# Performance work log

Measured on AMD Instinct MI355X. Metric: run time of the kernel, lower is better.

Reference implementation:

```python
import jax, jax.numpy as jnp
import numpy as np

B, N, D, P = 4, 16384, 128, 100


def setup_inputs() -> dict:
    key = jax.random.key(0)
    k1, k2, k3 = jax.random.split(key, 3)
    x = jax.random.normal(k1, (B, N, D), dtype=jnp.float32)
    y = jax.random.normal(k2, (B, N, D), dtype=jnp.float32)
    thetas = jax.random.normal(k3, (P, D), dtype=jnp.float32)
    return {"x": x, "y": y, "thetas": thetas}


def reference(x, y, thetas):
    # Sliced OT (the branch taken since B*N*N*4 bytes >> memory limit).
    n_proj = thetas.shape[0]
    # F.normalize(theta, dim=0) per projection direction (eps clamp 1e-12)
    norms = jnp.maximum(jnp.linalg.norm(thetas, axis=-1, keepdims=True), 1e-12)
    thetas = thetas / norms  # (P, d)

    # Project all points onto all directions: (P, B, N)
    x_proj = jnp.einsum('bnd,pd->pbn', x, thetas)
    y_proj = jnp.einsum('bnd,pd->pbn', y, thetas)

    # torch: sort y_proj; scatter y_sorted back to original order of x via
    # x_indices = argsort(x_proj). Equivalent: transported_proj[n] =
    # y_sorted[rank_of_x_proj[n]], with rank = argsort(argsort(.)).
    y_sorted = jnp.sort(y_proj, axis=-1)
    ranks = jnp.argsort(jnp.argsort(x_proj, axis=-1), axis=-1)
    transported_proj = jnp.take_along_axis(y_sorted, ranks, axis=-1)  # (P, B, N)

    # Accumulate (transported_proj - x_proj) * theta over projections.
    transported = jnp.einsum('pbn,pd->bnd', transported_proj - x_proj, thetas)
    return x + transported / n_proj
```

## Files before the change

kernel.cpp:

```cpp
#include <hip/hip_runtime.h>
#include <hip/hip_bf16.h>

#define B_    4
#define N_    16384
#define D_    128
#define P_    100
#define BN_   65536
#define PBN_  6553600
#define PPAD  112
#define KPAD  128
#define NBIN  4096

typedef __attribute__((ext_vector_type(8))) short short8;
typedef __attribute__((ext_vector_type(4))) float floatx4;

__device__ __forceinline__ unsigned short f2b(float f) {
    unsigned u = __float_as_uint(f);
    return (unsigned short)((u + 0x7FFFu + ((u >> 16) & 1u)) >> 16);
}
__device__ __forceinline__ float b2f(unsigned short h) {
    return __uint_as_float(((unsigned)h) << 16);
}

__global__ void k_norm(const float* __restrict__ th,
                       unsigned short* __restrict__ thb,
                       unsigned short* __restrict__ thbT) {
    int p = blockIdx.x;
    int d = threadIdx.x;
    float v = 0.f;
    if (p < P_) v = th[p * D_ + d];
    float s = v * v;
    #pragma unroll
    for (int o = 32; o > 0; o >>= 1) s += __shfl_down(s, o, 64);
    __shared__ float red[2];
    if ((d & 63) == 0) red[d >> 6] = s;
    __syncthreads();
    float norm = fmaxf(sqrtf(red[0] + red[1]), 1e-12f);
    unsigned short r = f2b(v / norm);
    if (p < PPAD) thb[p * D_ + d] = r;
    thbT[d * KPAD + p] = r;
}

__global__ __launch_bounds__(256, 4) void k_proj(
    const float* __restrict__ x, const float* __restrict__ y,
    const unsigned short* __restrict__ thb,
    unsigned short* __restrict__ xp, unsigned short* __restrict__ yp) {
    __shared__ unsigned short th_s[15232];
    __shared__ unsigned short buf[4608];
    const int tid  = threadIdx.x;
    const int w    = tid >> 6;
    const int lane = tid & 63;
    const int n    = lane & 15;
    const int quad = lane >> 4;
    const int row0 = blockIdx.x * 64;

    for (int g = tid; g < 1792; g += 256) {
        int r = g >> 4, c = (g & 15) << 3;
        *(uint4*)(th_s + r * 136 + c) = *(const uint4*)(thb + r * D_ + c);
    }

    const float* xr = x + (size_t)(row0 + w * 16 + n) * D_ + quad * 8;
    const float* yr = y + (size_t)(row0 + w * 16 + n) * D_ + quad * 8;
    short8 bx[4], by[4];
    {
        float4 lx[8];
        #pragma unroll
        for (int ks = 0; ks < 4; ++ks) {
            lx[2*ks]   = *(const float4*)(xr + ks * 32);
            lx[2*ks+1] = *(const float4*)(xr + ks * 32 + 4);
        }
        #pragma unroll
        for (int ks = 0; ks < 4; ++ks) {
            short8 t;
            t[0] = (short)f2b(lx[2*ks].x);   t[1] = (short)f2b(lx[2*ks].y);
            t[2] = (short)f2b(lx[2*ks].z);   t[3] = (short)f2b(lx[2*ks].w);
            t[4] = (short)f2b(lx[2*ks+1].x); t[5] = (short)f2b(lx[2*ks+1].y);
            t[6] = (short)f2b(lx[2*ks+1].z); t[7] = (short)f2b(lx[2*ks+1].w);
            bx[ks] = t;
        }
    }
    {
        float4 ly[8];
        #pragma unroll
        for (int ks = 0; ks < 4; ++ks) {
            ly[2*ks]   = *(const float4*)(yr + ks * 32);
            ly[2*ks+1] = *(const float4*)(yr + ks * 32 + 4);
        }
        #pragma unroll
        for (int ks = 0; ks < 4; ++ks) {
            short8 t;
            t[0] = (short)f2b(ly[2*ks].x);   t[1] = (short)f2b(ly[2*ks].y);
            t[2] = (short)f2b(ly[2*ks].z);   t[3] = (short)f2b(ly[2*ks].w);
            t[4] = (short)f2b(ly[2*ks+1].x); t[5] = (short)f2b(ly[2*ks+1].y);
            t[6] = (short)f2b(ly[2*ks+1].z); t[7] = (short)f2b(ly[2*ks+1].w);
            by[ks] = t;
        }
    }
    __syncthreads();

    floatx4 ay[7];

    #pragma unroll
    for (int pt = 0; pt < 4; ++pt) {
        floatx4 accx = {0.f, 0.f, 0.f, 0.f};
        floatx4 accy = {0.f, 0.f, 0.f, 0.f};
        #pragma unroll
        for (int ks = 0; ks < 4; ++ks) {
            short8 a = *(const short8*)(th_s + (pt * 16 + n) * 136 + ks * 32 + quad * 8);
            accx = __builtin_amdgcn_mfma_f32_16x16x32_bf16(a, bx[ks], accx, 0, 0, 0);
            accy = __builtin_amdgcn_mfma_f32_16x16x32_bf16(a, by[ks], accy, 0, 0, 0);
        }
        #pragma unroll
        for (int reg = 0; reg < 4; ++reg)
            buf[(pt * 16 + quad * 4 + reg) * 72 + w * 16 + n] = f2b(accx[reg]);
        ay[pt] = accy;
    }
    __syncthreads();
    for (int g = tid; g < 512; g += 256) {
        int p = g >> 3, c = (g & 7) << 3;
        *(uint4*)(xp + (size_t)p * BN_ + row0 + c) = *(const uint4*)(buf + p * 72 + c);
    }
    __syncthreads();

    #pragma unroll
    for (int pt = 4; pt < 7; ++pt) {
        floatx4 accx = {0.f, 0.f, 0.f, 0.f};
        floatx4 accy = {0.f, 0.f, 0.f, 0.f};
        #pragma unroll
        for (int ks = 0; ks < 4; ++ks) {
            short8 a = *(const short8*)(th_s + (pt * 16 + n) * 136 + ks * 32 + quad * 8);
            accx = __builtin_amdgcn_mfma_f32_16x16x32_bf16(a, bx[ks], accx, 0, 0, 0);
            accy = __builtin_amdgcn_mfma_f32_16x16x32_bf16(a, by[ks], accy, 0, 0, 0);
        }
        #pragma unroll
        for (int reg = 0; reg < 4; ++reg)
            buf[((pt - 4) * 16 + quad * 4 + reg) * 72 + w * 16 + n] = f2b(accx[reg]);
        ay[pt] = accy;
    }
    __syncthreads();
    for (int g = tid; g < 288; g += 256) {
        int p = g >> 3, c = (g & 7) << 3;
        *(uint4*)(xp + (size_t)(64 + p) * BN_ + row0 + c) = *(const uint4*)(buf + p * 72 + c);
    }
    __syncthreads();

    #pragma unroll
    for (int pt = 0; pt < 4; ++pt)
        #pragma unroll
        for (int reg = 0; reg < 4; ++reg)
            buf[(pt * 16 + quad * 4 + reg) * 72 + w * 16 + n] = f2b(ay[pt][reg]);
    __syncthreads();
    for (int g = tid; g < 512; g += 256) {
        int p = g >> 3, c = (g & 7) << 3;
        *(uint4*)(yp + (size_t)p * BN_ + row0 + c) = *(const uint4*)(buf + p * 72 + c);
    }
    __syncthreads();

    #pragma unroll
    for (int pt = 4; pt < 7; ++pt)
        #pragma unroll
        for (int reg = 0; reg < 4; ++reg)
            buf[((pt - 4) * 16 + quad * 4 + reg) * 72 + w * 16 + n] = f2b(ay[pt][reg]);
    __syncthreads();
    for (int g = tid; g < 288; g += 256) {
        int p = g >> 3, c = (g & 7) << 3;
        *(uint4*)(yp + (size_t)(64 + p) * BN_ + row0 + c) = *(const uint4*)(buf + p * 72 + c);
    }
}

__device__ __forceinline__ int binof(float v) {
    int k = (int)((v + 8.0f) * 256.0f);
    return k < 0 ? 0 : (k > NBIN - 1 ? NBIN - 1 : k);
}

__device__ __forceinline__ void scan4(unsigned* hist, volatile unsigned* wsum, int t) {
    unsigned v[4], run = 0;
    #pragma unroll
    for (int i = 0; i < 4; ++i) { unsigned h = hist[t * 4 + i]; v[i] = run; run += h; }
    const int lane = t & 63, w = t >> 6;
    unsigned inc = run;
    #pragma unroll
    for (int off = 1; off < 64; off <<= 1) {
        unsigned nbr = __shfl_up(inc, off, 64);
        if (lane >= off) inc += nbr;
    }
    if (lane == 63) wsum[w] = inc;
    __syncthreads();
    if (t == 0) {
        unsigned r2 = 0;
        #pragma unroll
        for (int i = 0; i < 16; ++i) { unsigned h = wsum[i]; wsum[i] = r2; r2 += h; }
    }
    __syncthreads();
    unsigned base = wsum[w] + (inc - run);
    #pragma unroll
    for (int i = 0; i < 4; ++i) hist[t * 4 + i] = base + v[i];
}

__global__ __launch_bounds__(1024, 8) void k_sortdiff(
    const unsigned short* __restrict__ xp, const unsigned short* __restrict__ yp,
    unsigned short* __restrict__ diff) {
    __shared__ unsigned hist[NBIN];
    __shared__ unsigned short ysort[N_];
    __shared__ unsigned wsum[16];
    const int t = threadIdx.x;
    const unsigned* ypd = (const unsigned*)(yp + (size_t)blockIdx.x * N_);
    const unsigned* xpd = (const unsigned*)(xp + (size_t)blockIdx.x * N_);
    unsigned*       dfd = (unsigned*)(diff + (size_t)blockIdx.x * N_);

    #pragma unroll
    for (int i = 0; i < 4; ++i) hist[t + i * 1024] = 0;
    __syncthreads();

    unsigned jy[8], jx[8];
    #pragma unroll
    for (int i = 0; i < 2; ++i) {
        uint4 a = *(const uint4*)(ypd + i * 4096 + t * 4);
        unsigned aw0 = a.x, aw1 = a.y, aw2 = a.z, aw3 = a.w;
        unsigned aws[4] = {aw0, aw1, aw2, aw3};
        #pragma unroll
        for (int q = 0; q < 4; ++q) {
            unsigned j0 = atomicAdd(&hist[binof(b2f((unsigned short)(aws[q] & 0xffff)))], 1u);
            unsigned j1 = atomicAdd(&hist[binof(b2f((unsigned short)(aws[q] >> 16)))], 1u);
            jy[4*i + q] = (j0 & 0xffffu) | (j1 << 16);
        }
    }
    #pragma unroll
    for (int i = 0; i < 2; ++i) {
        uint4 c = *(const uint4*)(xpd + i * 4096 + t * 4);
        unsigned cw0 = c.x, cw1 = c.y, cw2 = c.z, cw3 = c.w;
        unsigned cws[4] = {cw0, cw1, cw2, cw3};
        #pragma unroll
        for (int q = 0; q < 4; ++q) {
            unsigned i0 = atomicAdd(&hist[binof(b2f((unsigned short)(cws[q] & 0xffff)))], 0x10000u);
            unsigned i1 = atomicAdd(&hist[binof(b2f((unsigned short)(cws[q] >> 16)))], 0x10000u);
            jx[4*i + q] = (i0 >> 16) | (i1 & 0xffff0000u);
        }
    }
    __syncthreads();
    scan4(hist, wsum, t);
    __syncthreads();

    #pragma unroll
    for (int i = 0; i < 2; ++i) {
        uint4 a = *(const uint4*)(ypd + i * 4096 + t * 4);
        unsigned aws[4] = {a.x, a.y, a.z, a.w};
        #pragma unroll
        for (int q = 0; q < 4; ++q) {
            int k = 4*i + q;
            unsigned short e0 = (unsigned short)(aws[q] & 0xffff);
            unsigned short e1 = (unsigned short)(aws[q] >> 16);
            ysort[(hist[binof(b2f(e0))] & 0xffffu) + (jy[k] & 0xffffu)] = e0;
            ysort[(hist[binof(b2f(e1))] & 0xffffu) + (jy[k] >> 16)]     = e1;
        }
    }
    __syncthreads();

    #pragma unroll
    for (int i = 0; i < 2; ++i) {
        uint4 c = *(const uint4*)(xpd + i * 4096 + t * 4);
        unsigned cws[4] = {c.x, c.y, c.z, c.w};
        unsigned o[4];
        #pragma unroll
        for (int q = 0; q < 4; ++q) {
            int k = 4*i + q;
            float x0 = b2f((unsigned short)(cws[q] & 0xffff));
            float x1 = b2f((unsigned short)(cws[q] >> 16));
            unsigned r0 = (hist[binof(x0)] >> 16) + (jx[k] & 0xffffu);
            unsigned r1 = (hist[binof(x1)] >> 16) + (jx[k] >> 16);
            unsigned short d0 = f2b(b2f(ysort[r0]) - x0);
            unsigned short d1 = f2b(b2f(ysort[r1]) - x1);
            o[q] = (unsigned)d0 | ((unsigned)d1 << 16);
        }
        *(uint4*)(dfd + i * 4096 + t * 4) = make_uint4(o[0], o[1], o[2], o[3]);
    }
}

__global__ __launch_bounds__(256, 4) void k_comb(
    const float* __restrict__ x, const unsigned short* __restrict__ diff,
    const unsigned short* __restrict__ thbT, float* __restrict__ out) {
    __shared__ unsigned short ths[64 * 136];
    __shared__ unsigned Lp[64 * 68];
    const int tid  = threadIdx.x;
    const int w    = tid >> 6;
    const int lane = tid & 63;
    const int n16  = lane & 15;
    const int quad = lane >> 4;
    const int row0 = blockIdx.x * 64;

    for (int g = tid; g < 1024; g += 256) {
        int r = g >> 4, c = (g & 15) << 3;
        *(uint4*)(ths + r * 136 + c) = *(const uint4*)(thbT + r * KPAD + c);
    }
    for (int g = tid; g < 952; g += 256) Lp[50 * 68 + g] = 0;
    for (int g = tid; g < 400; g += 256) {
        int p2 = g >> 3, rg = (g & 7) << 3;
        uint4 a = *(const uint4*)(diff + (size_t)(2 * p2) * BN_ + row0 + rg);
        uint4 b = *(const uint4*)(diff + (size_t)(2 * p2 + 1) * BN_ + row0 + rg);
        unsigned* dst = Lp + p2 * 68 + rg;
        dst[0] = (a.x & 0xffffu) | (b.x << 16);
        dst[1] = (a.x >> 16)     | (b.x & 0xffff0000u);
        dst[2] = (a.y & 0xffffu) | (b.y << 16);
        dst[3] = (a.y >> 16)     | (b.y & 0xffff0000u);
        dst[4] = (a.z & 0xffffu) | (b.z << 16);
        dst[5] = (a.z >> 16)     | (b.z & 0xffff0000u);
        dst[6] = (a.w & 0xffffu) | (b.w << 16);
        dst[7] = (a.w >> 16)     | (b.w & 0xffff0000u);
    }
    __syncthreads();

    const int r = w * 16 + n16;
    short8 af[4];
    #pragma unroll
    for (int ks = 0; ks < 4; ++ks) {
        union { unsigned u[4]; short8 v; } tu;
        #pragma unroll
        for (int m = 0; m < 4; ++m)
            tu.u[m] = Lp[(ks * 16 + quad * 4 + m) * 68 + r];
        af[ks] = tu.v;
    }

    const float invP = 1.0f / (float)P_;
    const size_t rbase = (size_t)(row0 + w * 16 + quad * 4) * D_ + n16;

    #pragma unroll
    for (int nt = 0; nt < 4; ++nt) {
        floatx4 acc = {0.f, 0.f, 0.f, 0.f};
        #pragma unroll
        for (int ks = 0; ks < 4; ++ks) {
            short8 b = *(const short8*)(ths + (nt * 16 + n16) * 136 + ks * 32 + quad * 8);
            acc = __builtin_amdgcn_mfma_f32_16x16x32_bf16(af[ks], b, acc, 0, 0, 0);
        }
        #pragma unroll
        for (int reg = 0; reg < 4; ++reg) {
            size_t o = rbase + (size_t)reg * D_ + nt * 16;
            out[o] = fmaf(acc[reg], invP, x[o]);
        }
    }
    __syncthreads();

    for (int g = tid; g < 1024; g += 256) {
        int r2 = g >> 4, c = (g & 15) << 3;
        *(uint4*)(ths + r2 * 136 + c) = *(const uint4*)(thbT + (size_t)(64 + r2) * KPAD + c);
    }
    __syncthreads();

    #pragma unroll
    for (int nt = 0; nt < 4; ++nt) {
        floatx4 acc = {0.f, 0.f, 0.f, 0.f};
        #pragma unroll
        for (int ks = 0; ks < 4; ++ks) {
            short8 b = *(const short8*)(ths + (nt * 16 + n16) * 136 + ks * 32 + quad * 8);
            acc = __builtin_amdgcn_mfma_f32_16x16x32_bf16(af[ks], b, acc, 0, 0, 0);
        }
        #pragma unroll
        for (int reg = 0; reg < 4; ++reg) {
            size_t o = rbase + (size_t)reg * D_ + (64 + nt * 16);
            out[o] = fmaf(acc[reg], invP, x[o]);
        }
    }
}

extern "C" void kernel_launch(void* const* d_in, const int* in_sizes, int n_in,
                              void* d_out, int out_size, void* d_ws, size_t ws_size,
                              hipStream_t stream) {
    const float* x  = (const float*)d_in[0];
    const float* y  = (const float*)d_in[1];
    const float* th = (const float*)d_in[2];
    float* out = (float*)d_out;
    char*  wsb = (char*)d_ws;

    unsigned short* thb  = (unsigned short*)wsb;
    unsigned short* thbT = (unsigned short*)(wsb + 32768);
    unsigned short* xpb  = (unsigned short*)(wsb + 65536);
    unsigned short* ypb  = xpb + PBN_;

    k_norm<<<128, 128, 0, stream>>>(th, thb, thbT);
    k_proj<<<BN_ / 64, 256, 0, stream>>>(x, y, thb, xpb, ypb);
    k_sortdiff<<<P_ * B_, 1024, 0, stream>>>(xpb, ypb, xpb);
    k_comb<<<BN_ / 64, 256, 0, stream>>>(x, xpb, thbT, out);
}
```

Baseline: 138.3 us.

## Fuse theta normalization into projection kernel and drop separate norm launch

New measurement: 143.3 us. 3.6% more time.

```diff
diff --git a/kernel.cpp b/kernel.cpp
--- a/kernel.cpp
+++ b/kernel.cpp
@@ -22,31 +22,13 @@
     return __uint_as_float(((unsigned)h) << 16);
 }
 
-__global__ void k_norm(const float* __restrict__ th,
-                       unsigned short* __restrict__ thb,
-                       unsigned short* __restrict__ thbT) {
-    int p = blockIdx.x;
-    int d = threadIdx.x;
-    float v = 0.f;
-    if (p < P_) v = th[p * D_ + d];
-    float s = v * v;
-    #pragma unroll
-    for (int o = 32; o > 0; o >>= 1) s += __shfl_down(s, o, 64);
-    __shared__ float red[2];
-    if ((d & 63) == 0) red[d >> 6] = s;
-    __syncthreads();
-    float norm = fmaxf(sqrtf(red[0] + red[1]), 1e-12f);
-    unsigned short r = f2b(v / norm);
-    if (p < PPAD) thb[p * D_ + d] = r;
-    thbT[d * KPAD + p] = r;
-}
-
 __global__ __launch_bounds__(256, 4) void k_proj(
     const float* __restrict__ x, const float* __restrict__ y,
-    const unsigned short* __restrict__ thb,
+    const float* __restrict__ th, unsigned short* __restrict__ thbT,
     unsigned short* __restrict__ xp, unsigned short* __restrict__ yp) {
     __shared__ unsigned short th_s[15232];
     __shared__ unsigned short buf[4608];
+    __shared__ float invn[128];
     const int tid  = threadIdx.x;
     const int w    = tid >> 6;
     const int lane = tid & 63;
@@ -54,49 +36,72 @@
     const int quad = lane >> 4;
     const int row0 = blockIdx.x * 64;
 
+    const float* xr = x + (size_t)(row0 + w * 16 + n) * D_ + quad * 8;
+    const float* yr = y + (size_t)(row0 + w * 16 + n) * D_ + quad * 8;
+    float4 lx[8], ly[8];
+    #pragma unroll
+    for (int ks = 0; ks < 4; ++ks) {
+        lx[2*ks]   = *(const float4*)(xr + ks * 32);
+        lx[2*ks+1] = *(const float4*)(xr + ks * 32 + 4);
+        ly[2*ks]   = *(const float4*)(yr + ks * 32);
+        ly[2*ks+1] = *(const float4*)(yr + ks * 32 + 4);
+    }
+
+    {
+        int p = tid >> 1, half = tid & 1;
+        float s = 0.f;
+        if (p < P_) {
+            const float* tr = th + (size_t)p * D_ + half * 64;
+            #pragma unroll
+            for (int i = 0; i < 16; ++i) {
+                float4 v = *(const float4*)(tr + i * 4);
+                s += v.x * v.x + v.y * v.y + v.z * v.z + v.w * v.w;
+            }
+        }
+        s += __shfl_xor(s, 1, 64);
+        if (half == 0 && p < 128)
+            invn[p] = (p < P_) ? 1.f / fmaxf(sqrtf(s), 1e-12f) : 0.f;
+    }
+    __syncthreads();
+
     for (int g = tid; g < 1792; g += 256) {
         int r = g >> 4, c = (g & 15) << 3;
-        *(uint4*)(th_s + r * 136 + c) = *(const uint4*)(thb + r * D_ + c);
-    }
-
-    const float* xr = x + (size_t)(row0 + w * 16 + n) * D_ + quad * 8;
-    const float* yr = y + (size_t)(row0 + w * 16 + n) * D_ + quad * 8;
+        ushort4 lo, hi;
+        if (r < P_) {
+            float sc = invn[r];
+            float4 a = *(const float4*)(th + (size_t)r * D_ + c);
+            float4 b = *(const float4*)(th + (size_t)r * D_ + c + 4);
+            lo = make_ushort4(f2b(a.x * sc), f2b(a.y * sc), f2b(a.z * sc), f2b(a.w * sc));
+            hi = make_ushort4(f2b(b.x * sc), f2b(b.y * sc), f2b(b.z * sc), f2b(b.w * sc));
+        } else {
+            lo = make_ushort4(0, 0, 0, 0);
+            hi = make_ushort4(0, 0, 0, 0);
+        }
+        *(ushort4*)(th_s + r * 136 + c)     = lo;
+        *(ushort4*)(th_s + r * 136 + c + 4) = hi;
+    }
+    __syncthreads();
+
+    if (blockIdx.x < KPAD && tid < KPAD) {
+        int d = blockIdx.x;
+        unsigned short v = (tid < PPAD) ? th_s[tid * 136 + d] : (unsigned short)0;
+        thbT[(size_t)d * KPAD + tid] = v;
+    }
+
     short8 bx[4], by[4];
-    {
-        float4 lx[8];
-        #pragma unroll
-        for (int ks = 0; ks < 4; ++ks) {
-            lx[2*ks]   = *(const float4*)(xr + ks * 32);
-            lx[2*ks+1] = *(const float4*)(xr + ks * 32 + 4);
-        }
-        #pragma unroll
-        for (int ks = 0; ks < 4; ++ks) {
-            short8 t;
-            t[0] = (short)f2b(lx[2*ks].x);   t[1] = (short)f2b(lx[2*ks].y);
-            t[2] = (short)f2b(lx[2*ks].z);   t[3] = (short)f2b(lx[2*ks].w);
-            t[4] = (short)f2b(lx[2*ks+1].x); t[5] = (short)f2b(lx[2*ks+1].y);
-            t[6] = (short)f2b(lx[2*ks+1].z); t[7] = (short)f2b(lx[2*ks+1].w);
-            bx[ks] = t;
-        }
-    }
-    {
-        float4 ly[8];
-        #pragma unroll
-        for (int ks = 0; ks < 4; ++ks) {
-            ly[2*ks]   = *(const float4*)(yr + ks * 32);
-            ly[2*ks+1] = *(const float4*)(yr + ks * 32 + 4);
-        }
-        #pragma unroll
-        for (int ks = 0; ks < 4; ++ks) {
-            short8 t;
-            t[0] = (short)f2b(ly[2*ks].x);   t[1] = (short)f2b(ly[2*ks].y);
-            t[2] = (short)f2b(ly[2*ks].z);   t[3] = (short)f2b(ly[2*ks].w);
-            t[4] = (short)f2b(ly[2*ks+1].x); t[5] = (short)f2b(ly[2*ks+1].y);
-            t[6] = (short)f2b(ly[2*ks+1].z); t[7] = (short)f2b(ly[2*ks+1].w);
-            by[ks] = t;
-        }
-    }
-    __syncthreads();
+    #pragma unroll
+    for (int ks = 0; ks < 4; ++ks) {
+        short8 tx, ty;
+        tx[0] = (short)f2b(lx[2*ks].x);   ty[0] = (short)f2b(ly[2*ks].x);
+        tx[1] = (short)f2b(lx[2*ks].y);   ty[1] = (short)f2b(ly[2*ks].y);
+        tx[2] = (short)f2b(lx[2*ks].z);   ty[2] = (short)f2b(ly[2*ks].z);
+        tx[3] = (short)f2b(lx[2*ks].w);   ty[3] = (short)f2b(ly[2*ks].w);
+        tx[4] = (short)f2b(lx[2*ks+1].x); ty[4] = (short)f2b(ly[2*ks+1].x);
+        tx[5] = (short)f2b(lx[2*ks+1].y); ty[5] = (short)f2b(ly[2*ks+1].y);
+        tx[6] = (short)f2b(lx[2*ks+1].z); ty[6] = (short)f2b(ly[2*ks+1].z);
+        tx[7] = (short)f2b(lx[2*ks+1].w); ty[7] = (short)f2b(ly[2*ks+1].w);
+        bx[ks] = tx; by[ks] = ty;
+    }
 
     floatx4 ay[7];
 
@@ -216,8 +221,7 @@
     #pragma unroll
     for (int i = 0; i < 2; ++i) {
         uint4 a = *(const uint4*)(ypd + i * 4096 + t * 4);
-        unsigned aw0 = a.x, aw1 = a.y, aw2 = a.z, aw3 = a.w;
-        unsigned aws[4] = {aw0, aw1, aw2, aw3};
+        unsigned aws[4] = {a.x, a.y, a.z, a.w};
         #pragma unroll
         for (int q = 0; q < 4; ++q) {
             unsigned j0 = atomicAdd(&hist[binof(b2f((unsigned short)(aws[q] & 0xffff)))], 1u);
@@ -228,8 +232,7 @@
     #pragma unroll
     for (int i = 0; i < 2; ++i) {
         uint4 c = *(const uint4*)(xpd + i * 4096 + t * 4);
-        unsigned cw0 = c.x, cw1 = c.y, cw2 = c.z, cw3 = c.w;
-        unsigned cws[4] = {cw0, cw1, cw2, cw3};
+        unsigned cws[4] = {c.x, c.y, c.z, c.w};
         #pragma unroll
         for (int q = 0; q < 4; ++q) {
             unsigned i0 = atomicAdd(&hist[binof(b2f((unsigned short)(cws[q] & 0xffff)))], 0x10000u);
@@ -370,13 +373,11 @@
     float* out = (float*)d_out;
     char*  wsb = (char*)d_ws;
 
-    unsigned short* thb  = (unsigned short*)wsb;
     unsigned short* thbT = (unsigned short*)(wsb + 32768);
     unsigned short* xpb  = (unsigned short*)(wsb + 65536);
     unsigned short* ypb  = xpb + PBN_;
 
-    k_norm<<<128, 128, 0, stream>>>(th, thb, thbT);
-    k_proj<<<BN_ / 64, 256, 0, stream>>>(x, y, thb, xpb, ypb);
+    k_proj<<<BN_ / 64, 256, 0, stream>>>(x, y, th, thbT, xpb, ypb);
     k_sortdiff<<<P_ * B_, 1024, 0, stream>>>(xpb, ypb, xpb);
     k_comb<<<BN_ / 64, 256, 0, stream>>>(x, xpb, thbT, out);
 }
```
